# Kernel tuning notes

Hardware: AMD Instinct MI355X
Metric: run time of the kernel (lower is better)

## Reference

```python
import jax, jax.numpy as jnp
import numpy as np

RADIUS = 0.4
K = 32
EPS = 1e-5


def ball_query(xyz, new_xyz, radius, k):
    """xyz: (B,N,3), new_xyz: (B,M,3) -> idx (B,M,k) int32.
    Replicates CUDA ball_query: first k points within radius (in index order),
    padded with the first found index."""
    N = xyz.shape[1]
    # squared distances (B,M,N)
    d2 = jnp.sum((new_xyz[:, :, None, :] - xyz[:, None, :, :]) ** 2, axis=-1)
    within = d2 < radius * radius
    order = jnp.arange(N, dtype=jnp.int32)
    key = jnp.where(within, order[None, None, :], N)
    idx_sorted = jnp.argsort(key, axis=-1)[..., :k].astype(jnp.int32)  # (B,M,k)
    cnt = within.sum(axis=-1)  # (B,M)
    first = idx_sorted[..., :1]
    slot = jnp.arange(k)[None, None, :]
    return jnp.where(slot < cnt[..., None], idx_sorted, first)


def gather_bmk(x_bnc, idx):
    """x_bnc: (B,N,C), idx: (B,M,K) -> (B,M,K,C)"""
    return jnp.take_along_axis(x_bnc[:, None, :, :], idx[..., None], axis=2)


def conv_bn_relu(x, w, b, gamma, beta):
    """x: (B,Cin,M,K); w: (Cout,Cin). 1x1 Conv2d + BatchNorm2d (train stats) + ReLU."""
    x = jnp.einsum('bcmk,oc->bomk', x, w) + b[None, :, None, None]
    mu = x.mean(axis=(0, 2, 3), keepdims=True)
    var = x.var(axis=(0, 2, 3), keepdims=True)
    x = gamma[None, :, None, None] * (x - mu) * jax.lax.rsqrt(var + EPS) + beta[None, :, None, None]
    return jax.nn.relu(x)


def setup_inputs() -> dict:
    key = jax.random.key(0)
    ks = jax.random.split(key, 16)
    B, N, C, M = 4, 16384, 128, 1024
    mlp = [131, 128, 128, 256]
    inp = {
        'points_xyz': jax.random.normal(ks[0], (B, N, 3), dtype=jnp.float32),
        'features': jax.random.normal(ks[1], (B, C, N), dtype=jnp.float32),
        'indices': jax.random.randint(ks[2], (B, M), 0, N, dtype=jnp.int32),
    }
    for i in range(3):
        cin, cout = mlp[i], mlp[i + 1]
        inp[f'w{i+1}'] = jax.random.normal(ks[3 + 4 * i], (cout, cin), dtype=jnp.float32) / np.sqrt(cin)
        inp[f'b{i+1}'] = jnp.zeros((cout,), dtype=jnp.float32)
        inp[f'g{i+1}'] = jnp.ones((cout,), dtype=jnp.float32)
        inp[f'beta{i+1}'] = jnp.zeros((cout,), dtype=jnp.float32)
    return inp


def reference(points_xyz, features, indices,
              w1, b1, g1, beta1, w2, b2, g2, beta2, w3, b3, g3, beta3):
    # sample centers: new_xyz (B,M,3)
    new_xyz = jnp.take_along_axis(points_xyz, indices[..., None], axis=1)
    # ball query + group
    idx = ball_query(points_xyz, new_xyz, RADIUS, K)            # (B,M,K)
    grouped_xyz = gather_bmk(points_xyz, idx) - new_xyz[:, :, None, :]  # (B,M,K,3)
    grouped_feat = gather_bmk(features.transpose(0, 2, 1), idx)         # (B,M,K,C)
    x = jnp.concatenate([grouped_xyz, grouped_feat], axis=-1)           # (B,M,K,3+C)
    x = x.transpose(0, 3, 1, 2)                                         # (B,3+C,M,K)
    # shared MLP (1x1 Conv2d + BN + ReLU)
    x = conv_bn_relu(x, w1, b1, g1, beta1)
    x = conv_bn_relu(x, w2, b2, g2, beta2)
    x = conv_bn_relu(x, w3, b3, g3, beta3)
    # max pool over K -> (B, Cout, M)
    new_features = x.max(axis=-1)
    return new_xyz, new_features
```

## Files before the change

### kernel.cpp

```cpp
#include <hip/hip_runtime.h>

#define B_ 4
#define N_ 16384
#define C_ 128
#define M_ 1024
#define K_ 32
#define NTOT (B_*M_*K_)
#define RAD2 0.16f
#define EPS_ 1e-5f

typedef unsigned short ushort_t;
typedef __bf16 bf16x8 __attribute__((ext_vector_type(8)));
typedef float f32x4 __attribute__((ext_vector_type(4)));

__device__ __forceinline__ float b2f(ushort_t u){
  unsigned int x = ((unsigned int)u) << 16;
  return __builtin_bit_cast(float, x);
}
__device__ __forceinline__ ushort_t f2b(float f){
  return __builtin_bit_cast(ushort_t, (__bf16)f);
}

__global__ __launch_bounds__(256) void prep_all_k(
    const float* __restrict__ feat, ushort_t* __restrict__ ftr_t,
    const float* __restrict__ xyz, const int* __restrict__ indices,
    float* __restrict__ new_xyz, int* __restrict__ idx,
    const float* __restrict__ w1, const float* __restrict__ w2, const float* __restrict__ w3,
    ushort_t* __restrict__ W1b, ushort_t* __restrict__ W2b, ushort_t* __restrict__ W3b,
    float* __restrict__ stats)
{
  __shared__ float T[32][133];
  int bid = blockIdx.x;
  int t = threadIdx.x;

  if (bid < 1024){
    int wv = t >> 6, lane = t & 63;
    int g = bid*4 + wv;
    int b = g >> 10;
    const float* pb = xyz + (size_t)b*N_*3;
    const float4* pb4 = (const float4*)pb;
    int qi = indices[g];
    float qx = pb[qi*3+0], qy = pb[qi*3+1], qz = pb[qi*3+2];
    if (lane < 3) new_xyz[g*3 + lane] = pb[qi*3 + lane];

    int cnt = 0, firstIdx = 0;
    int* op = idx + g*K_;

    float4 buf0[6], buf1[6];
    #pragma unroll
    for (int i = 0; i < 6; i++) buf0[i] = pb4[lane*6 + i];

    unsigned long long below = (lane == 0) ? 0ull : ((~0ull) >> (64 - lane));

    auto process = [&](const float4* buf, int chunk){
      const float* f = (const float*)buf;
      unsigned int local_mask = 0;
      #pragma unroll
      for (int j = 0; j < 8; j++){
        float dx = f[j*3+0]-qx, dy = f[j*3+1]-qy, dz = f[j*3+2]-qz;
        if (dx*dx + dy*dy + dz*dz < RAD2) local_mask |= (1u << j);
      }
      unsigned long long many = __ballot(local_mask != 0);
      if (many == 0ull) return;
      int base = chunk*512;
      unsigned long long mj[8];
      #pragma unroll
      for (int j = 0; j < 8; j++) mj[j] = __ballot((local_mask >> j) & 1u);
      int excl = 0, total = 0;
      #pragma unroll
      for (int j = 0; j < 8; j++){
        excl  += __popcll(mj[j] & below);
        total += __popcll(mj[j]);
      }
      if (cnt == 0){
        int l0 = __builtin_ctzll(many);
        int j0 = 0;
        #pragma unroll
        for (int j = 7; j >= 0; j--) if ((mj[j] >> l0) & 1ull) j0 = j;
        firstIdx = base + l0*8 + j0;
      }
      int sl = cnt + excl;
      unsigned int m = local_mask;
      while (m && sl < K_){
        int j = __builtin_ctz(m); m &= m - 1u;
        op[sl++] = base + lane*8 + j;
      }
      cnt += total;
    };

    for (int chunk = 0; chunk < 32; chunk += 2){
      if (chunk + 1 < 32){
        #pragma unroll
        for (int i = 0; i < 6; i++) buf1[i] = pb4[(chunk+1)*384 + lane*6 + i];
      }
      process(buf0, chunk);
      if (cnt >= K_) break;
      if (chunk + 2 < 32){
        #pragma unroll
        for (int i = 0; i < 6; i++) buf0[i] = pb4[(chunk+2)*384 + lane*6 + i];
      }
      process(buf1, chunk + 1);
      if (cnt >= K_) break;
    }
    if (cnt < K_){
      for (int s = cnt + lane; s < K_; s += 64) op[s] = firstIdx;
    }
  } else if (bid < 3072){
    int bb = bid - 1024;
    int b = bb >> 9, ntile = bb & 511;
    int n0 = ntile * 32;
    int nl = t & 31;
    #pragma unroll
    for (int ci = 0; ci < 16; ci++){
      int c = ci*8 + (t >> 5);
      T[nl][c] = feat[((size_t)b*C_ + c)*N_ + n0 + nl];
    }
    __syncthreads();
    #pragma unroll
    for (int ii = 0; ii < 2; ii++){
      int v = ii*256 + t;
      int n2 = v >> 4, seg = v & 15;
      union { ushort_t u[8]; uint4 q; } pk;
      #pragma unroll
      for (int j = 0; j < 8; j++) pk.u[j] = f2b(T[n2][seg*8 + j]);
      *(uint4*)(ftr_t + ((size_t)b*N_ + n0 + n2)*C_ + seg*8) = pk.q;
    }
  } else {
    const int T1 = 128*160, T2 = 128*128;
    int e = (bid - 3072)*256 + t;
    if (e < T1){
      int o = e / 160, c = e % 160;
      float v = 0.f;
      if (c < 128) v = w1[o*131 + 3 + c];
      else if (c < 131) v = w1[o*131 + (c - 128)];
      W1b[e] = f2b(v);
    } else if (e < T1+T2){
      int e2 = e - T1;
      W2b[e2] = f2b(w2[e2]);
    } else {
      int e3 = e - T1 - T2;
      W3b[e3] = f2b(w3[e3]);
    }
    if (bid == 3072){
      #pragma unroll
      for (int j = 0; j < 6; j++) stats[j*256 + t] = 0.f;
    }
  }
}

__global__ __launch_bounds__(256, 4) void conv1_k(
    const float* __restrict__ xyz, const ushort_t* __restrict__ ftr_t,
    const int* __restrict__ idx, const float* __restrict__ new_xyz,
    const ushort_t* __restrict__ W1b, const float* __restrict__ b1,
    ushort_t* __restrict__ Y1, float* __restrict__ sumO, float* __restrict__ sqO)
{
  __shared__ alignas(16) ushort_t Xs[2][32*168];
  __shared__ alignas(16) float Ys[2][32*68];
  int t = threadIdx.x;
  int wv = t >> 6, lane = t & 63, quad = lane >> 4, l15 = lane & 15;
  int row = t >> 3, chunk = t & 7;
  int col0 = (blockIdx.x & 1) * 64;
  int blk = blockIdx.x >> 1;

  if (t < 128){
    int rr = t >> 2, cc = t & 3;
    *(uint4*)(Xs[0] + rr*168 + 128 + cc*8) = make_uint4(0,0,0,0);
    *(uint4*)(Xs[1] + rr*168 + 128 + cc*8) = make_uint4(0,0,0,0);
  }
  bf16x8 wf[5];
  #pragma unroll
  for (int kt = 0; kt < 5; kt++)
    wf[kt] = *(const bf16x8*)(W1b + (col0 + wv*16 + l15)*160 + kt*32 + quad*8);
  float bs_r = b1[col0 + wv*16 + l15];
  float s = 0.f, s2 = 0.f;

  const int GPB = 8;
  int g0 = blk * GPB;
  int b = g0 >> 10;
  int ia[GPB], ibv[GPB];
  #pragma unroll
  for (int i = 0; i < GPB; i++){
    ia[i]  = idx[(g0+i)*K_ + row];
    ibv[i] = idx[(g0+i)*K_ + (t & 31)];
  }
  uint4 r0, r1;
  float p3x, p3y, p3z, q3x, q3y, q3z;
  {
    const ushort_t* src = ftr_t + ((size_t)b*N_ + ia[0])*C_ + chunk*16;
    r0 = *(const uint4*)src; r1 = *(const uint4*)(src + 8);
    if (t < 32){
      const float* pp = xyz + ((size_t)b*N_ + ibv[0])*3;
      const float* qq = new_xyz + (size_t)g0*3;
      p3x = pp[0]; p3y = pp[1]; p3z = pp[2];
      q3x = qq[0]; q3y = qq[1]; q3z = qq[2];
    }
  }
  for (int i = 0; i < GPB; i++){
    int p = i & 1;
    ushort_t* X = Xs[p];
    *(uint4*)(X + row*168 + chunk*16) = r0;
    *(uint4*)(X + row*168 + chunk*16 + 8) = r1;
    if (t < 32){
      unsigned int u0 = (unsigned int)f2b(p3x-q3x) | ((unsigned int)f2b(p3y-q3y) << 16);
      unsigned int u1 = (unsigned int)f2b(p3z-q3z);
      *(uint2*)(X + t*168 + 128) = make_uint2(u0, u1);
    }
    if (i + 1 < GPB){
      const ushort_t* src = ftr_t + ((size_t)b*N_ + ia[i+1])*C_ + chunk*16;
      r0 = *(const uint4*)src; r1 = *(const uint4*)(src + 8);
      if (t < 32){
        const float* pp = xyz + ((size_t)b*N_ + ibv[i+1])*3;
        const float* qq = new_xyz + (size_t)(g0+i+1)*3;
        p3x = pp[0]; p3y = pp[1]; p3z = pp[2];
        q3x = qq[0]; q3y = qq[1]; q3z = qq[2];
      }
    }
    __syncthreads();
    bf16x8 af[2][5];
    #pragma unroll
    for (int mt = 0; mt < 2; mt++)
      #pragma unroll
      for (int kt = 0; kt < 5; kt++)
        af[mt][kt] = *(const bf16x8*)(X + (mt*16 + l15)*168 + kt*32 + quad*8);
    f32x4 acc[2] = {(f32x4){0,0,0,0}, (f32x4){0,0,0,0}};
    #pragma unroll
    for (int kt = 0; kt < 5; kt++){
      acc[0] = __builtin_amdgcn_mfma_f32_16x16x32_bf16(af[0][kt], wf[kt], acc[0], 0,0,0);
      acc[1] = __builtin_amdgcn_mfma_f32_16x16x32_bf16(af[1][kt], wf[kt], acc[1], 0,0,0);
    }
    {
      int o = wv*16 + l15;
      float* Yw = Ys[p];
      #pragma unroll
      for (int mt = 0; mt < 2; mt++)
        #pragma unroll
        for (int r = 0; r < 4; r++){
          float v = acc[mt][r] + bs_r;
          s += v; s2 += v*v;
          Yw[(mt*16 + quad*4 + r)*68 + o] = v;
        }
    }
    if (i > 0){
      const float* yp = &Ys[p^1][row*68 + chunk*8];
      f32x4 y0 = *(const f32x4*)(yp);
      f32x4 y1 = *(const f32x4*)(yp + 4);
      union { ushort_t u[8]; uint4 q; } p0;
      #pragma unroll
      for (int j = 0; j < 4; j++){
        p0.u[j] = f2b(y0[j]); p0.u[4+j] = f2b(y1[j]);
      }
      *(uint4*)(Y1 + ((size_t)(g0+i-1)*K_ + row)*128 + col0 + chunk*8) = p0.q;
    }
  }
  __syncthreads();
  {
    const float* yp = &Ys[(GPB-1)&1][row*68 + chunk*8];
    f32x4 y0 = *(const f32x4*)(yp);
    f32x4 y1 = *(const f32x4*)(yp + 4);
    union { ushort_t u[8]; uint4 q; } p0;
    #pragma unroll
    for (int j = 0; j < 4; j++){
      p0.u[j] = f2b(y0[j]); p0.u[4+j] = f2b(y1[j]);
    }
    *(uint4*)(Y1 + ((size_t)(g0+GPB-1)*K_ + row)*128 + col0 + chunk*8) = p0.q;
  }
  s  += __shfl_xor(s, 16);  s  += __shfl_xor(s, 32);
  s2 += __shfl_xor(s2, 16); s2 += __shfl_xor(s2, 32);
  if (quad == 0){
    int o = col0 + wv*16 + l15;
    atomicAdd(&sumO[o], s);
    atomicAdd(&sqO[o], s2);
  }
}

template<int COUT, bool MAXMIN, int MINB>
__global__ __launch_bounds__(256, MINB) void convB_k(
    const ushort_t* __restrict__ Yin, const ushort_t* __restrict__ Wb,
    const float* __restrict__ bias, const float* __restrict__ g_bn,
    const float* __restrict__ beta_bn, const float* __restrict__ sumI,
    const float* __restrict__ sqI, ushort_t* __restrict__ Yout,
    unsigned int* __restrict__ Ymm, float* __restrict__ sumO, float* __restrict__ sqO)
{
  constexpr int HALF = COUT/2;
  constexpr int NT = HALF/64;
  __shared__ alignas(16) ushort_t Xs[2][32*136];
  __shared__ alignas(16) float Ys[MAXMIN ? 1 : 2][MAXMIN ? 4 : 32*68];
  int t = threadIdx.x;
  int wv = t >> 6, lane = t & 63, quad = lane >> 4, l15 = lane & 15;
  int row = t >> 3, chunk = t & 7;
  int col0 = (blockIdx.x & 1) * HALF;
  int blk = blockIdx.x >> 1;

  float a_r[16], d_r[16];
  #pragma unroll
  for (int j = 0; j < 16; j++){
    int c = chunk*16 + j;
    float mu  = sumI[c] * (1.f/NTOT);
    float var = sqI[c]  * (1.f/NTOT) - mu*mu;
    float a = g_bn[c] * rsqrtf(var + EPS_);
    a_r[j] = a; d_r[j] = beta_bn[c] - a*mu;
  }
  bf16x8 wf[NT][4];
  #pragma unroll
  for (int nt = 0; nt < NT; nt++)
    #pragma unroll
    for (int kt = 0; kt < 4; kt++)
      wf[nt][kt] = *(const bf16x8*)(Wb + (col0 + wv*(NT*16) + nt*16 + l15)*128 + kt*32 + quad*8);
  float bs_r[NT];
  #pragma unroll
  for (int nt = 0; nt < NT; nt++) bs_r[nt] = bias[col0 + wv*(NT*16) + nt*16 + l15];
  float s[NT], s2[NT];
  #pragma unroll
  for (int nt = 0; nt < NT; nt++){ s[nt] = 0.f; s2[nt] = 0.f; }

  const int GPB = 8;
  int g0 = blk * GPB;
  uint4 r0, r1;
  {
    const ushort_t* src = Yin + ((size_t)g0*K_ + row)*128 + chunk*16;
    r0 = *(const uint4*)src; r1 = *(const uint4*)(src + 8);
  }
  for (int i = 0; i < GPB; i++){
    int p = i & 1;
    int g = g0 + i;
    ushort_t* X = Xs[p];
    union { ushort_t u[8]; uint4 q; } i0, i1, o0, o1;
    i0.q = r0; i1.q = r1;
    #pragma unroll
    for (int j = 0; j < 8; j++){
      o0.u[j] = f2b(fmaxf(a_r[j]  *b2f(i0.u[j]) + d_r[j],   0.f));
      o1.u[j] = f2b(fmaxf(a_r[8+j]*b2f(i1.u[j]) + d_r[8+j], 0.f));
    }
    *(uint4*)(X + row*136 + chunk*16) = o0.q;
    *(uint4*)(X + row*136 + chunk*16 + 8) = o1.q;
    if (i + 1 < GPB){
      const ushort_t* src = Yin + ((size_t)(g+1)*K_ + row)*128 + chunk*16;
      r0 = *(const uint4*)src; r1 = *(const uint4*)(src + 8);
    }
    __syncthreads();
    bf16x8 af[2][4];
    #pragma unroll
    for (int mt = 0; mt < 2; mt++)
      #pragma unroll
      for (int kt = 0; kt < 4; kt++)
        af[mt][kt] = *(const bf16x8*)(X + (mt*16 + l15)*136 + kt*32 + quad*8);
    f32x4 acc[NT][2];
    #pragma unroll
    for (int nt = 0; nt < NT; nt++){ acc[nt][0] = (f32x4){0,0,0,0}; acc[nt][1] = (f32x4){0,0,0,0}; }
    #pragma unroll
    for (int nt = 0; nt < NT; nt++)
      #pragma unroll
      for (int kt = 0; kt < 4; kt++){
        acc[nt][0] = __builtin_amdgcn_mfma_f32_16x16x32_bf16(af[0][kt], wf[nt][kt], acc[nt][0], 0,0,0);
        acc[nt][1] = __builtin_amdgcn_mfma_f32_16x16x32_bf16(af[1][kt], wf[nt][kt], acc[nt][1], 0,0,0);
      }
    if constexpr (!MAXMIN){
      {
        int o = wv*16 + l15;
        float* Yw = Ys[p];
        #pragma unroll
        for (int mt = 0; mt < 2; mt++)
          #pragma unroll
          for (int r = 0; r < 4; r++){
            float v = acc[0][mt][r] + bs_r[0];
            s[0] += v; s2[0] += v*v;
            Yw[(mt*16 + quad*4 + r)*68 + o] = v;
          }
      }
      if (i > 0){
        const float* yp = &Ys[p^1][row*68 + chunk*8];
        f32x4 y0 = *(const f32x4*)(yp);
        f32x4 y1 = *(const f32x4*)(yp + 4);
        union { ushort_t u[8]; uint4 q; } p0;
        #pragma unroll
        for (int j = 0; j < 4; j++){
          p0.u[j] = f2b(y0[j]); p0.u[4+j] = f2b(y1[j]);
        }
        *(uint4*)(Yout + ((size_t)(g-1)*K_ + row)*128 + col0 + chunk*8) = p0.q;
      }
    } else {
      #pragma unroll
      for (int nt = 0; nt < NT; nt++){
        float v0 = acc[nt][0][0] + bs_r[nt];
        float mx = v0, mn = v0;
        s[nt] += v0; s2[nt] += v0*v0;
        #pragma unroll
        for (int mt = 0; mt < 2; mt++)
          #pragma unroll
          for (int r = 0; r < 4; r++){
            if (mt == 0 && r == 0) continue;
            float v = acc[nt][mt][r] + bs_r[nt];
            s[nt] += v; s2[nt] += v*v;
            mx = fmaxf(mx, v); mn = fminf(mn, v);
          }
        mx = fmaxf(mx, __shfl_xor(mx, 16)); mx = fmaxf(mx, __shfl_xor(mx, 32));
        mn = fminf(mn, __shfl_xor(mn, 16)); mn = fminf(mn, __shfl_xor(mn, 32));
        if (quad == 0){
          int o = col0 + wv*(NT*16) + nt*16 + l15;
          Ymm[(size_t)g*256 + o] = (unsigned int)f2b(mx) | ((unsigned int)f2b(mn) << 16);
        }
      }
    }
  }
  if constexpr (!MAXMIN){
    __syncthreads();
    const float* yp = &Ys[(GPB-1)&1][row*68 + chunk*8];
    f32x4 y0 = *(const f32x4*)(yp);
    f32x4 y1 = *(const f32x4*)(yp + 4);
    union { ushort_t u[8]; uint4 q; } p0;
    #pragma unroll
    for (int j = 0; j < 4; j++){
      p0.u[j] = f2b(y0[j]); p0.u[4+j] = f2b(y1[j]);
    }
    *(uint4*)(Yout + ((size_t)(g0+GPB-1)*K_ + row)*128 + col0 + chunk*8) = p0.q;
  }
  #pragma unroll
  for (int nt = 0; nt < NT; nt++){
    s[nt]  += __shfl_xor(s[nt], 16);  s[nt]  += __shfl_xor(s[nt], 32);
    s2[nt] += __shfl_xor(s2[nt], 16); s2[nt] += __shfl_xor(s2[nt], 32);
    if (quad == 0){
      int o = col0 + wv*(NT*16) + nt*16 + l15;
      atomicAdd(&sumO[o], s[nt]);
      atomicAdd(&sqO[o], s2[nt]);
    }
  }
}

__global__ __launch_bounds__(256) void finalize_k(
    const unsigned int* __restrict__ Ymm, const float* __restrict__ g3,
    const float* __restrict__ beta3, const float* __restrict__ sum3,
    const float* __restrict__ sq3, float* __restrict__ out)
{
  __shared__ float T[16][264];
  __shared__ float abn[256], dbn[256];
  int t = threadIdx.x;
  int b = blockIdx.x >> 6;
  int m0 = (blockIdx.x & 63) * 16;
  {
    float mu  = sum3[t] * (1.f/NTOT);
    float var = sq3[t]  * (1.f/NTOT) - mu*mu;
    float a = g3[t] * rsqrtf(var + EPS_);
    abn[t] = a; dbn[t] = beta3[t] - a*mu;
  }
  __syncthreads();
  #pragma unroll
  for (int i = 0; i < 4; i++){
    int v4 = i*256 + t;
    int m = v4 >> 6, oq = (v4 & 63) * 4;
    uint4 w = *(const uint4*)(Ymm + ((size_t)(b*M_ + m0 + m))*256 + oq);
    unsigned int wsv[4] = {w.x, w.y, w.z, w.w};
    float r[4];
    #pragma unroll
    for (int j = 0; j < 4; j++){
      int o = oq + j;
      float mx = b2f((ushort_t)(wsv[j] & 0xffffu));
      float mn = b2f((ushort_t)(wsv[j] >> 16));
      float a = abn[o];
      float val = (a >= 0.f) ? (a*mx + dbn[o]) : (a*mn + dbn[o]);
      r[j] = fmaxf(val, 0.f);
    }
    *(f32x4*)(&T[m][oq]) = *(f32x4*)r;
  }
  __syncthreads();
  #pragma unroll
  for (int p = 0; p < 4; p++){
    int o = p*64 + (t >> 2), c = t & 3;
    float4 v = make_float4(T[c*4+0][o], T[c*4+1][o], T[c*4+2][o], T[c*4+3][o]);
    *(float4*)(out + ((size_t)(b*256 + o))*M_ + m0 + c*4) = v;
  }
}

extern "C" void kernel_launch(void* const* d_in, const int* in_sizes, int n_in,
                              void* d_out, int out_size, void* d_ws, size_t ws_size,
                              hipStream_t stream)
{
  (void)in_sizes; (void)n_in; (void)out_size; (void)ws_size;
  const float* xyz  = (const float*)d_in[0];
  const float* feat = (const float*)d_in[1];
  const int*   inds = (const int*)d_in[2];
  const float* w1 = (const float*)d_in[3];
  const float* b1 = (const float*)d_in[4];
  const float* g1 = (const float*)d_in[5];
  const float* be1= (const float*)d_in[6];
  const float* w2 = (const float*)d_in[7];
  const float* b2 = (const float*)d_in[8];
  const float* g2 = (const float*)d_in[9];
  const float* be2= (const float*)d_in[10];
  const float* w3 = (const float*)d_in[11];
  const float* b3 = (const float*)d_in[12];
  const float* g3 = (const float*)d_in[13];
  const float* be3= (const float*)d_in[14];

  char* ws = (char*)d_ws;
  float* stats = (float*)ws;
  float* s1sum = stats + 0*256;  float* s1sq = stats + 1*256;
  float* s2sum = stats + 2*256;  float* s2sq = stats + 3*256;
  float* s3sum = stats + 4*256;  float* s3sq = stats + 5*256;
  size_t off = 6*256*sizeof(float);
  int* idx = (int*)(ws + off);                off += (size_t)B_*M_*K_*4;
  ushort_t* ftr_t = (ushort_t*)(ws + off);    off += (size_t)B_*N_*C_*2;
  ushort_t* W1b = (ushort_t*)(ws + off);      off += 128*160*2;
  ushort_t* W2b = (ushort_t*)(ws + off);      off += 128*128*2;
  ushort_t* W3b = (ushort_t*)(ws + off);      off += 256*128*2;
  ushort_t* Y1 = (ushort_t*)(ws + off);       off += (size_t)NTOT*128*2;
  ushort_t* Y2 = (ushort_t*)(ws + off);       off += (size_t)NTOT*128*2;
  unsigned int* Ymm = (unsigned int*)(ws + off); off += (size_t)B_*M_*256*4;

  float* new_xyz  = (float*)d_out;
  float* out_feat = (float*)d_out + (size_t)B_*M_*3;

  prep_all_k<<<3344, 256, 0, stream>>>(feat, ftr_t, xyz, inds, new_xyz, idx,
                                       w1, w2, w3, W1b, W2b, W3b, stats);
  conv1_k<<<1024, 256, 0, stream>>>(xyz, ftr_t, idx, new_xyz, W1b, b1, Y1, s1sum, s1sq);
  convB_k<128,false,4><<<1024, 256, 0, stream>>>(Y1, W2b, b2, g1, be1, s1sum, s1sq, Y2, nullptr, s2sum, s2sq);
  convB_k<256,true ,3><<<1024, 256, 0, stream>>>(Y2, W3b, b3, g2, be2, s2sum, s2sq, nullptr, Ymm, s3sum, s3sq);
  finalize_k<<<256, 256, 0, stream>>>(Ymm, g3, be3, s3sum, s3sq, out_feat);
}
```

Measured before the change: 211.6 us.

## Store conv2 output in MFMA fragment layout and split conv2/conv3 kernels

Conv2 now computes all 128 output channels per block over 4 groups and writes its results straight from MFMA accumulators in a fragment-native layout. This drops the LDS staging buffer and the transpose pass that came before the global write. Conv3 reads that layout and rebuilds the row-major LDS tile with per-channel-pair BN+ReLU, then keeps the max/min epilogue. The aim is to cut LDS traffic and syncs in conv2, at the cost of narrower scattered 8-byte stores and more scattered LDS writes in conv3.

```diff
diff --git a/kernel.cpp b/kernel.cpp
--- a/kernel.cpp
+++ b/kernel.cpp
@@ -273,23 +273,18 @@
   }
 }
 
-template<int COUT, bool MAXMIN, int MINB>
-__global__ __launch_bounds__(256, MINB) void convB_k(
+__global__ __launch_bounds__(256, 4) void conv2_k(
     const ushort_t* __restrict__ Yin, const ushort_t* __restrict__ Wb,
     const float* __restrict__ bias, const float* __restrict__ g_bn,
     const float* __restrict__ beta_bn, const float* __restrict__ sumI,
-    const float* __restrict__ sqI, ushort_t* __restrict__ Yout,
-    unsigned int* __restrict__ Ymm, float* __restrict__ sumO, float* __restrict__ sqO)
+    const float* __restrict__ sqI, ushort_t* __restrict__ Yf,
+    float* __restrict__ sumO, float* __restrict__ sqO)
 {
-  constexpr int HALF = COUT/2;
-  constexpr int NT = HALF/64;
   __shared__ alignas(16) ushort_t Xs[2][32*136];
-  __shared__ alignas(16) float Ys[MAXMIN ? 1 : 2][MAXMIN ? 4 : 32*68];
   int t = threadIdx.x;
   int wv = t >> 6, lane = t & 63, quad = lane >> 4, l15 = lane & 15;
   int row = t >> 3, chunk = t & 7;
-  int col0 = (blockIdx.x & 1) * HALF;
-  int blk = blockIdx.x >> 1;
+  int blk = blockIdx.x;
 
   float a_r[16], d_r[16];
   #pragma unroll
@@ -300,20 +295,18 @@
     float a = g_bn[c] * rsqrtf(var + EPS_);
     a_r[j] = a; d_r[j] = beta_bn[c] - a*mu;
   }
-  bf16x8 wf[NT][4];
-  #pragma unroll
-  for (int nt = 0; nt < NT; nt++)
+  bf16x8 wf[2][4];
+  #pragma unroll
+  for (int nt = 0; nt < 2; nt++)
     #pragma unroll
     for (int kt = 0; kt < 4; kt++)
-      wf[nt][kt] = *(const bf16x8*)(Wb + (col0 + wv*(NT*16) + nt*16 + l15)*128 + kt*32 + quad*8);
-  float bs_r[NT];
-  #pragma unroll
-  for (int nt = 0; nt < NT; nt++) bs_r[nt] = bias[col0 + wv*(NT*16) + nt*16 + l15];
-  float s[NT], s2[NT];
-  #pragma unroll
-  for (int nt = 0; nt < NT; nt++){ s[nt] = 0.f; s2[nt] = 0.f; }
-
-  const int GPB = 8;
+      wf[nt][kt] = *(const bf16x8*)(Wb + (wv*32 + nt*16 + l15)*128 + kt*32 + quad*8);
+  float bs_r[2];
+  #pragma unroll
+  for (int nt = 0; nt < 2; nt++) bs_r[nt] = bias[wv*32 + nt*16 + l15];
+  float s[2] = {0.f, 0.f}, s2[2] = {0.f, 0.f};
+
+  const int GPB = 4;
   int g0 = blk * GPB;
   uint4 r0, r1;
   {
@@ -338,88 +331,152 @@
       r0 = *(const uint4*)src; r1 = *(const uint4*)(src + 8);
     }
     __syncthreads();
-    bf16x8 af[2][4];
-    #pragma unroll
-    for (int mt = 0; mt < 2; mt++)
-      #pragma unroll
-      for (int kt = 0; kt < 4; kt++)
-        af[mt][kt] = *(const bf16x8*)(X + (mt*16 + l15)*136 + kt*32 + quad*8);
-    f32x4 acc[NT][2];
-    #pragma unroll
-    for (int nt = 0; nt < NT; nt++){ acc[nt][0] = (f32x4){0,0,0,0}; acc[nt][1] = (f32x4){0,0,0,0}; }
-    #pragma unroll
-    for (int nt = 0; nt < NT; nt++)
-      #pragma unroll
-      for (int kt = 0; kt < 4; kt++){
-        acc[nt][0] = __builtin_amdgcn_mfma_f32_16x16x32_bf16(af[0][kt], wf[nt][kt], acc[nt][0], 0,0,0);
-        acc[nt][1] = __builtin_amdgcn_mfma_f32_16x16x32_bf16(af[1][kt], wf[nt][kt], acc[nt][1], 0,0,0);
-      }
-    if constexpr (!MAXMIN){
-      {
-        int o = wv*16 + l15;
-        float* Yw = Ys[p];
-        #pragma unroll
-        for (int mt = 0; mt < 2; mt++)
-          #pragma unroll
-          for (int r = 0; r < 4; r++){
-            float v = acc[0][mt][r] + bs_r[0];
-            s[0] += v; s2[0] += v*v;
-            Yw[(mt*16 + quad*4 + r)*68 + o] = v;
-          }
-      }
-      if (i > 0){
-        const float* yp = &Ys[p^1][row*68 + chunk*8];
-        f32x4 y0 = *(const f32x4*)(yp);
-        f32x4 y1 = *(const f32x4*)(yp + 4);
-        union { ushort_t u[8]; uint4 q; } p0;
-        #pragma unroll
-        for (int j = 0; j < 4; j++){
-          p0.u[j] = f2b(y0[j]); p0.u[4+j] = f2b(y1[j]);
-        }
-        *(uint4*)(Yout + ((size_t)(g-1)*K_ + row)*128 + col0 + chunk*8) = p0.q;
-      }
-    } else {
-      #pragma unroll
-      for (int nt = 0; nt < NT; nt++){
-        float v0 = acc[nt][0][0] + bs_r[nt];
-        float mx = v0, mn = v0;
-        s[nt] += v0; s2[nt] += v0*v0;
-        #pragma unroll
-        for (int mt = 0; mt < 2; mt++)
-          #pragma unroll
-          for (int r = 0; r < 4; r++){
-            if (mt == 0 && r == 0) continue;
-            float v = acc[nt][mt][r] + bs_r[nt];
-            s[nt] += v; s2[nt] += v*v;
-            mx = fmaxf(mx, v); mn = fminf(mn, v);
-          }
-        mx = fmaxf(mx, __shfl_xor(mx, 16)); mx = fmaxf(mx, __shfl_xor(mx, 32));
-        mn = fminf(mn, __shfl_xor(mn, 16)); mn = fminf(mn, __shfl_xor(mn, 32));
-        if (quad == 0){
-          int o = col0 + wv*(NT*16) + nt*16 + l15;
-          Ymm[(size_t)g*256 + o] = (unsigned int)f2b(mx) | ((unsigned int)f2b(mn) << 16);
-        }
-      }
-    }
-  }
-  if constexpr (!MAXMIN){
-    __syncthreads();
-    const float* yp = &Ys[(GPB-1)&1][row*68 + chunk*8];
-    f32x4 y0 = *(const f32x4*)(yp);
-    f32x4 y1 = *(const f32x4*)(yp + 4);
-    union { ushort_t u[8]; uint4 q; } p0;
-    #pragma unroll
-    for (int j = 0; j < 4; j++){
-      p0.u[j] = f2b(y0[j]); p0.u[4+j] = f2b(y1[j]);
-    }
-    *(uint4*)(Yout + ((size_t)(g0+GPB-1)*K_ + row)*128 + col0 + chunk*8) = p0.q;
-  }
-  #pragma unroll
-  for (int nt = 0; nt < NT; nt++){
+    f32x4 acc[2][2];
+    acc[0][0] = (f32x4){0,0,0,0}; acc[0][1] = (f32x4){0,0,0,0};
+    acc[1][0] = (f32x4){0,0,0,0}; acc[1][1] = (f32x4){0,0,0,0};
+    #pragma unroll
+    for (int kt = 0; kt < 4; kt++){
+      bf16x8 A0 = *(const bf16x8*)(X + (l15)*136      + kt*32 + quad*8);
+      bf16x8 A1 = *(const bf16x8*)(X + (16 + l15)*136 + kt*32 + quad*8);
+      acc[0][0] = __builtin_amdgcn_mfma_f32_16x16x32_bf16(A0, wf[0][kt], acc[0][0], 0,0,0);
+      acc[0][1] = __builtin_amdgcn_mfma_f32_16x16x32_bf16(A1, wf[0][kt], acc[0][1], 0,0,0);
+      acc[1][0] = __builtin_amdgcn_mfma_f32_16x16x32_bf16(A0, wf[1][kt], acc[1][0], 0,0,0);
+      acc[1][1] = __builtin_amdgcn_mfma_f32_16x16x32_bf16(A1, wf[1][kt], acc[1][1], 0,0,0);
+    }
+    #pragma unroll
+    for (int nt = 0; nt < 2; nt++){
+      #pragma unroll
+      for (int mt = 0; mt < 2; mt++){
+        float v0 = acc[nt][mt][0] + bs_r[nt];
+        float v1 = acc[nt][mt][1] + bs_r[nt];
+        float v2 = acc[nt][mt][2] + bs_r[nt];
+        float v3 = acc[nt][mt][3] + bs_r[nt];
+        s[nt]  += v0 + v1 + v2 + v3;
+        s2[nt] += v0*v0 + v1*v1 + v2*v2 + v3*v3;
+        uint2 w;
+        w.x = (unsigned int)f2b(v0) | ((unsigned int)f2b(v1) << 16);
+        w.y = (unsigned int)f2b(v2) | ((unsigned int)f2b(v3) << 16);
+        size_t seg = ((size_t)g*2 + mt)*8 + (wv*2 + nt);
+        *(uint2*)(Yf + seg*256 + (quad*16 + l15)*4) = w;
+      }
+    }
+  }
+  #pragma unroll
+  for (int nt = 0; nt < 2; nt++){
     s[nt]  += __shfl_xor(s[nt], 16);  s[nt]  += __shfl_xor(s[nt], 32);
     s2[nt] += __shfl_xor(s2[nt], 16); s2[nt] += __shfl_xor(s2[nt], 32);
     if (quad == 0){
-      int o = col0 + wv*(NT*16) + nt*16 + l15;
+      int o = wv*32 + nt*16 + l15;
+      atomicAdd(&sumO[o], s[nt]);
+      atomicAdd(&sqO[o], s2[nt]);
+    }
+  }
+}
+
+__global__ __launch_bounds__(256, 4) void conv3_k(
+    const ushort_t* __restrict__ Yf, const ushort_t* __restrict__ Wb,
+    const float* __restrict__ bias, const float* __restrict__ g_bn,
+    const float* __restrict__ beta_bn, const float* __restrict__ sumI,
+    const float* __restrict__ sqI,
+    unsigned int* __restrict__ Ymm, float* __restrict__ sumO, float* __restrict__ sqO)
+{
+  __shared__ alignas(16) ushort_t Xs[2][32*136];
+  int t = threadIdx.x;
+  int wv = t >> 6, lane = t & 63, quad = lane >> 4, l15 = lane & 15;
+  int col0 = (blockIdx.x & 1) * 128;
+  int blk = blockIdx.x >> 1;
+
+  int rest = t & 255;
+  int sseg = rest >> 5, q = (rest >> 3) & 3, pr = rest & 7;
+  int c0 = sseg*16 + pr*2;
+  float A0c, D0c, A1c, D1c;
+  {
+    float mu0  = sumI[c0] * (1.f/NTOT);
+    float var0 = sqI[c0]  * (1.f/NTOT) - mu0*mu0;
+    A0c = g_bn[c0] * rsqrtf(var0 + EPS_);
+    D0c = beta_bn[c0] - A0c*mu0;
+    float mu1  = sumI[c0+1] * (1.f/NTOT);
+    float var1 = sqI[c0+1]  * (1.f/NTOT) - mu1*mu1;
+    A1c = g_bn[c0+1] * rsqrtf(var1 + EPS_);
+    D1c = beta_bn[c0+1] - A1c*mu1;
+  }
+  bf16x8 wf[2][4];
+  #pragma unroll
+  for (int nt = 0; nt < 2; nt++)
+    #pragma unroll
+    for (int kt = 0; kt < 4; kt++)
+      wf[nt][kt] = *(const bf16x8*)(Wb + (col0 + wv*32 + nt*16 + l15)*128 + kt*32 + quad*8);
+  float bs_r[2];
+  #pragma unroll
+  for (int nt = 0; nt < 2; nt++) bs_r[nt] = bias[col0 + wv*32 + nt*16 + l15];
+  float s[2] = {0.f, 0.f}, s2[2] = {0.f, 0.f};
+
+  const int GPB = 8;
+  int g0 = blk * GPB;
+  int finner = sseg*256 + q*64 + pr*8;
+  uint4 r0, r1;
+  r0 = *(const uint4*)(Yf + ((size_t)g0*2 + 0)*2048 + finner);
+  r1 = *(const uint4*)(Yf + ((size_t)g0*2 + 1)*2048 + finner);
+  for (int i = 0; i < GPB; i++){
+    int p = i & 1;
+    int g = g0 + i;
+    ushort_t* X = Xs[p];
+    union { ushort_t u[8]; uint4 q4; } i0, i1;
+    i0.q4 = r0; i1.q4 = r1;
+    #pragma unroll
+    for (int r = 0; r < 4; r++){
+      unsigned int w0 = (unsigned int)f2b(fmaxf(A0c*b2f(i0.u[r])   + D0c, 0.f))
+                      | ((unsigned int)f2b(fmaxf(A1c*b2f(i0.u[4+r]) + D1c, 0.f)) << 16);
+      unsigned int w1 = (unsigned int)f2b(fmaxf(A0c*b2f(i1.u[r])   + D0c, 0.f))
+                      | ((unsigned int)f2b(fmaxf(A1c*b2f(i1.u[4+r]) + D1c, 0.f)) << 16);
+      *(unsigned int*)(X + (q*4 + r)*136 + c0)      = w0;
+      *(unsigned int*)(X + (16 + q*4 + r)*136 + c0) = w1;
+    }
+    if (i + 1 < GPB){
+      r0 = *(const uint4*)(Yf + ((size_t)(g+1)*2 + 0)*2048 + finner);
+      r1 = *(const uint4*)(Yf + ((size_t)(g+1)*2 + 1)*2048 + finner);
+    }
+    __syncthreads();
+    f32x4 acc[2][2];
+    acc[0][0] = (f32x4){0,0,0,0}; acc[0][1] = (f32x4){0,0,0,0};
+    acc[1][0] = (f32x4){0,0,0,0}; acc[1][1] = (f32x4){0,0,0,0};
+    #pragma unroll
+    for (int kt = 0; kt < 4; kt++){
+      bf16x8 A0 = *(const bf16x8*)(X + (l15)*136      + kt*32 + quad*8);
+      bf16x8 A1 = *(const bf16x8*)(X + (16 + l15)*136 + kt*32 + quad*8);
+      acc[0][0] = __builtin_amdgcn_mfma_f32_16x16x32_bf16(A0, wf[0][kt], acc[0][0], 0,0,0);
+      acc[0][1] = __builtin_amdgcn_mfma_f32_16x16x32_bf16(A1, wf[0][kt], acc[0][1], 0,0,0);
+      acc[1][0] = __builtin_amdgcn_mfma_f32_16x16x32_bf16(A0, wf[1][kt], acc[1][0], 0,0,0);
+      acc[1][1] = __builtin_amdgcn_mfma_f32_16x16x32_bf16(A1, wf[1][kt], acc[1][1], 0,0,0);
+    }
+    #pragma unroll
+    for (int nt = 0; nt < 2; nt++){
+      float v0 = acc[nt][0][0] + bs_r[nt];
+      float mx = v0, mn = v0;
+      s[nt] += v0; s2[nt] += v0*v0;
+      #pragma unroll
+      for (int mt = 0; mt < 2; mt++)
+        #pragma unroll
+        for (int r = 0; r < 4; r++){
+          if (mt == 0 && r == 0) continue;
+          float v = acc[nt][mt][r] + bs_r[nt];
+          s[nt] += v; s2[nt] += v*v;
+          mx = fmaxf(mx, v); mn = fminf(mn, v);
+        }
+      mx = fmaxf(mx, __shfl_xor(mx, 16)); mx = fmaxf(mx, __shfl_xor(mx, 32));
+      mn = fminf(mn, __shfl_xor(mn, 16)); mn = fminf(mn, __shfl_xor(mn, 32));
+      if (quad == 0){
+        int o = col0 + wv*32 + nt*16 + l15;
+        Ymm[(size_t)g*256 + o] = (unsigned int)f2b(mx) | ((unsigned int)f2b(mn) << 16);
+      }
+    }
+  }
+  #pragma unroll
+  for (int nt = 0; nt < 2; nt++){
+    s[nt]  += __shfl_xor(s[nt], 16);  s[nt]  += __shfl_xor(s[nt], 32);
+    s2[nt] += __shfl_xor(s2[nt], 16); s2[nt] += __shfl_xor(s2[nt], 32);
+    if (quad == 0){
+      int o = col0 + wv*32 + nt*16 + l15;
       atomicAdd(&sumO[o], s[nt]);
       atomicAdd(&sqO[o], s2[nt]);
     }
@@ -512,7 +569,7 @@
   prep_all_k<<<3344, 256, 0, stream>>>(feat, ftr_t, xyz, inds, new_xyz, idx,
                                        w1, w2, w3, W1b, W2b, W3b, stats);
   conv1_k<<<1024, 256, 0, stream>>>(xyz, ftr_t, idx, new_xyz, W1b, b1, Y1, s1sum, s1sq);
-  convB_k<128,false,4><<<1024, 256, 0, stream>>>(Y1, W2b, b2, g1, be1, s1sum, s1sq, Y2, nullptr, s2sum, s2sq);
-  convB_k<256,true ,3><<<1024, 256, 0, stream>>>(Y2, W3b, b3, g2, be2, s2sum, s2sq, nullptr, Ymm, s3sum, s3sq);
+  conv2_k<<<1024, 256, 0, stream>>>(Y1, W2b, b2, g1, be1, s1sum, s1sq, Y2, s2sum, s2sq);
+  conv3_k<<<1024, 256, 0, stream>>>(Y2, W3b, b3, g2, be2, s2sum, s2sq, Ymm, s3sum, s3sq);
   finalize_k<<<256, 256, 0, stream>>>(Ymm, g3, be3, s3sum, s3sq, out_feat);
 }
```

Result: slower. 220.2 us (+4.1%).

## Stage ball-query points through shared memory in SoA layout shared by block

Applied to the files above, without the earlier changes.

The ball-query block now loads each 512-point chunk once cooperatively into a double-buffered SoA shared-memory arena, instead of each wave loading its own float4 slices from global memory. The four waves in a block share the xyz chunks and synchronize each step, leaving the loop together once all waves have found K neighbors. Point assignment now interleaves lanes (point j*64+lane), and the per-lane output loop is replaced by a per-bit prefix scheme. This cuts redundant global loads across waves, but adds block-wide barriers that make early-finishing waves wait for the slowest one.

```diff
diff --git a/kernel.cpp b/kernel.cpp
--- a/kernel.cpp
+++ b/kernel.cpp
@@ -38,69 +38,82 @@
     int g = bid*4 + wv;
     int b = g >> 10;
     const float* pb = xyz + (size_t)b*N_*3;
-    const float4* pb4 = (const float4*)pb;
     int qi = indices[g];
     float qx = pb[qi*3+0], qy = pb[qi*3+1], qz = pb[qi*3+2];
     if (lane < 3) new_xyz[g*3 + lane] = pb[qi*3 + lane];
 
     int cnt = 0, firstIdx = 0;
     int* op = idx + g*K_;
-
-    float4 buf0[6], buf1[6];
-    #pragma unroll
-    for (int i = 0; i < 6; i++) buf0[i] = pb4[lane*6 + i];
-
     unsigned long long below = (lane == 0) ? 0ull : ((~0ull) >> (64 - lane));
 
-    auto process = [&](const float4* buf, int chunk){
-      const float* f = (const float*)buf;
+    float* arena = &T[0][0];
+    int sp[6], sc[6];
+    #pragma unroll
+    for (int k = 0; k < 6; k++){
+      int f = t + k*256;
+      sp[k] = f / 3; sc[k] = f - sp[k]*3;
+    }
+
+    float ld[6];
+    auto stageLoad = [&](int c){
+      const float* src = pb + c*1536;
+      #pragma unroll
+      for (int k = 0; k < 6; k++) ld[k] = src[t + k*256];
+    };
+    auto stageWrite = [&](int buf){
+      float* A = arena + buf*1536;
+      #pragma unroll
+      for (int k = 0; k < 6; k++) A[sc[k]*512 + sp[k]] = ld[k];
+    };
+
+    auto process = [&](int buf, int c){
+      const float* AX = arena + buf*1536;
+      const float* AY = AX + 512;
+      const float* AZ = AY + 512;
       unsigned int local_mask = 0;
       #pragma unroll
       for (int j = 0; j < 8; j++){
-        float dx = f[j*3+0]-qx, dy = f[j*3+1]-qy, dz = f[j*3+2]-qz;
+        int p = j*64 + lane;
+        float dx = AX[p]-qx, dy = AY[p]-qy, dz = AZ[p]-qz;
         if (dx*dx + dy*dy + dz*dz < RAD2) local_mask |= (1u << j);
       }
       unsigned long long many = __ballot(local_mask != 0);
       if (many == 0ull) return;
-      int base = chunk*512;
+      int base = c*512;
       unsigned long long mj[8];
       #pragma unroll
       for (int j = 0; j < 8; j++) mj[j] = __ballot((local_mask >> j) & 1u);
-      int excl = 0, total = 0;
+      if (cnt == 0){
+        int j0 = 7;
+        #pragma unroll
+        for (int j = 7; j >= 0; j--) if (mj[j] != 0ull) j0 = j;
+        firstIdx = base + j0*64 + __builtin_ctzll(mj[j0]);
+      }
+      int pref = 0;
       #pragma unroll
       for (int j = 0; j < 8; j++){
-        excl  += __popcll(mj[j] & below);
-        total += __popcll(mj[j]);
-      }
-      if (cnt == 0){
-        int l0 = __builtin_ctzll(many);
-        int j0 = 0;
-        #pragma unroll
-        for (int j = 7; j >= 0; j--) if ((mj[j] >> l0) & 1ull) j0 = j;
-        firstIdx = base + l0*8 + j0;
-      }
-      int sl = cnt + excl;
-      unsigned int m = local_mask;
-      while (m && sl < K_){
-        int j = __builtin_ctz(m); m &= m - 1u;
-        op[sl++] = base + lane*8 + j;
-      }
-      cnt += total;
+        if ((local_mask >> j) & 1u){
+          int sl = cnt + pref + __popcll(mj[j] & below);
+          if (sl < K_) op[sl] = base + j*64 + lane;
+        }
+        pref += __popcll(mj[j]);
+      }
+      cnt += pref;
     };
 
-    for (int chunk = 0; chunk < 32; chunk += 2){
-      if (chunk + 1 < 32){
-        #pragma unroll
-        for (int i = 0; i < 6; i++) buf1[i] = pb4[(chunk+1)*384 + lane*6 + i];
-      }
-      process(buf0, chunk);
-      if (cnt >= K_) break;
-      if (chunk + 2 < 32){
-        #pragma unroll
-        for (int i = 0; i < 6; i++) buf0[i] = pb4[(chunk+2)*384 + lane*6 + i];
-      }
-      process(buf1, chunk + 1);
-      if (cnt >= K_) break;
+    stageLoad(0);
+    stageWrite(0);
+    __syncthreads();
+    bool wdone = false;
+    for (int c = 0; c < 32; c++){
+      bool have_next = (c + 1 < 32);
+      if (have_next) stageLoad(c + 1);
+      if (!wdone){
+        process(c & 1, c);
+        if (cnt >= K_) wdone = true;
+      }
+      if (have_next) stageWrite((c + 1) & 1);
+      if (__syncthreads_and((int)wdone)) break;
     }
     if (cnt < K_){
       for (int s = cnt + lane; s < K_; s += 64) op[s] = firstIdx;
```

Result: slower. 219.3 us (+3.6%).

## Add dedicated conv2 kernel covering all 128 output channels per block

Applied to the files above, without the earlier changes.

Replaces the generic convB kernel for layer 2 with a specialised kernel where each block computes all 128 output channels for 4 groups. Each wave keeps a 32-channel weight slice in registers and loads, normalises and activates the input tile once, where the generic kernel appears to split output channels into halves. Group processing is double-buffered in shared memory, so the next group's input load and the previous group's bf16 output store overlap with the current MFMA work. The cost is more registers and shared memory per block, which may reduce occupancy.

```diff
diff --git a/kernel.cpp b/kernel.cpp
--- a/kernel.cpp
+++ b/kernel.cpp
@@ -270,6 +270,142 @@
     int o = col0 + wv*16 + l15;
     atomicAdd(&sumO[o], s);
     atomicAdd(&sqO[o], s2);
+  }
+}
+
+__global__ __launch_bounds__(256, 3) void conv2_k(
+    const ushort_t* __restrict__ Yin, const ushort_t* __restrict__ Wb,
+    const float* __restrict__ bias, const float* __restrict__ g_bn,
+    const float* __restrict__ beta_bn, const float* __restrict__ sumI,
+    const float* __restrict__ sqI, ushort_t* __restrict__ Yout,
+    float* __restrict__ sumO, float* __restrict__ sqO)
+{
+  __shared__ alignas(16) ushort_t Xs[2][32*136];
+  __shared__ alignas(16) float Ys[2][32*132];
+  int t = threadIdx.x;
+  int wv = t >> 6, lane = t & 63, quad = lane >> 4, l15 = lane & 15;
+  int row = t >> 3, chunk = t & 7;
+  int blk = blockIdx.x;
+
+  float a_r[16], d_r[16];
+  #pragma unroll
+  for (int j = 0; j < 16; j++){
+    int c = chunk*16 + j;
+    float mu  = sumI[c] * (1.f/NTOT);
+    float var = sqI[c]  * (1.f/NTOT) - mu*mu;
+    float a = g_bn[c] * rsqrtf(var + EPS_);
+    a_r[j] = a; d_r[j] = beta_bn[c] - a*mu;
+  }
+  bf16x8 wf[2][4];
+  #pragma unroll
+  for (int nt = 0; nt < 2; nt++)
+    #pragma unroll
+    for (int kt = 0; kt < 4; kt++)
+      wf[nt][kt] = *(const bf16x8*)(Wb + (wv*32 + nt*16 + l15)*128 + kt*32 + quad*8);
+  float bs_r[2];
+  #pragma unroll
+  for (int nt = 0; nt < 2; nt++) bs_r[nt] = bias[wv*32 + nt*16 + l15];
+  float s[2] = {0.f, 0.f}, s2[2] = {0.f, 0.f};
+
+  const int GPB = 4;
+  int g0 = blk * GPB;
+  uint4 r0, r1;
+  {
+    const ushort_t* src = Yin + ((size_t)g0*K_ + row)*128 + chunk*16;
+    r0 = *(const uint4*)src; r1 = *(const uint4*)(src + 8);
+  }
+  for (int i = 0; i < GPB; i++){
+    int p = i & 1;
+    int g = g0 + i;
+    ushort_t* X = Xs[p];
+    union { ushort_t u[8]; uint4 q; } i0, i1, o0, o1;
+    i0.q = r0; i1.q = r1;
+    #pragma unroll
+    for (int j = 0; j < 8; j++){
+      o0.u[j] = f2b(fmaxf(a_r[j]  *b2f(i0.u[j]) + d_r[j],   0.f));
+      o1.u[j] = f2b(fmaxf(a_r[8+j]*b2f(i1.u[j]) + d_r[8+j], 0.f));
+    }
+    *(uint4*)(X + row*136 + chunk*16) = o0.q;
+    *(uint4*)(X + row*136 + chunk*16 + 8) = o1.q;
+    if (i + 1 < GPB){
+      const ushort_t* src = Yin + ((size_t)(g+1)*K_ + row)*128 + chunk*16;
+      r0 = *(const uint4*)src; r1 = *(const uint4*)(src + 8);
+    }
+    __syncthreads();
+    bf16x8 af[2][4];
+    #pragma unroll
+    for (int mt = 0; mt < 2; mt++)
+      #pragma unroll
+      for (int kt = 0; kt < 4; kt++)
+        af[mt][kt] = *(const bf16x8*)(X + (mt*16 + l15)*136 + kt*32 + quad*8);
+    f32x4 acc[2][2];
+    acc[0][0] = (f32x4){0,0,0,0}; acc[0][1] = (f32x4){0,0,0,0};
+    acc[1][0] = (f32x4){0,0,0,0}; acc[1][1] = (f32x4){0,0,0,0};
+    #pragma unroll
+    for (int kt = 0; kt < 4; kt++){
+      acc[0][0] = __builtin_amdgcn_mfma_f32_16x16x32_bf16(af[0][kt], wf[0][kt], acc[0][0], 0,0,0);
+      acc[0][1] = __builtin_amdgcn_mfma_f32_16x16x32_bf16(af[1][kt], wf[0][kt], acc[0][1], 0,0,0);
+      acc[1][0] = __builtin_amdgcn_mfma_f32_16x16x32_bf16(af[0][kt], wf[1][kt], acc[1][0], 0,0,0);
+      acc[1][1] = __builtin_amdgcn_mfma_f32_16x16x32_bf16(af[1][kt], wf[1][kt], acc[1][1], 0,0,0);
+    }
+    {
+      float* Yw = Ys[p];
+      #pragma unroll
+      for (int nt = 0; nt < 2; nt++){
+        int o = wv*32 + nt*16 + l15;
+        #pragma unroll
+        for (int mt = 0; mt < 2; mt++)
+          #pragma unroll
+          for (int r = 0; r < 4; r++){
+            float v = acc[nt][mt][r] + bs_r[nt];
+            s[nt] += v; s2[nt] += v*v;
+            Yw[(mt*16 + quad*4 + r)*132 + o] = v;
+          }
+      }
+    }
+    if (i > 0){
+      const float* yp = &Ys[p^1][row*132 + chunk*16];
+      f32x4 y0 = *(const f32x4*)(yp);
+      f32x4 y1 = *(const f32x4*)(yp + 4);
+      f32x4 y2 = *(const f32x4*)(yp + 8);
+      f32x4 y3 = *(const f32x4*)(yp + 12);
+      union { ushort_t u[16]; uint4 q[2]; } p0;
+      #pragma unroll
+      for (int j = 0; j < 4; j++){
+        p0.u[j]    = f2b(y0[j]); p0.u[4+j]  = f2b(y1[j]);
+        p0.u[8+j]  = f2b(y2[j]); p0.u[12+j] = f2b(y3[j]);
+      }
+      ushort_t* dst = Yout + ((size_t)(g-1)*K_ + row)*128 + chunk*16;
+      *(uint4*)dst = p0.q[0];
+      *(uint4*)(dst + 8) = p0.q[1];
+    }
+  }
+  __syncthreads();
+  {
+    const float* yp = &Ys[(GPB-1)&1][row*132 + chunk*16];
+    f32x4 y0 = *(const f32x4*)(yp);
+    f32x4 y1 = *(const f32x4*)(yp + 4);
+    f32x4 y2 = *(const f32x4*)(yp + 8);
+    f32x4 y3 = *(const f32x4*)(yp + 12);
+    union { ushort_t u[16]; uint4 q[2]; } p0;
+    #pragma unroll
+    for (int j = 0; j < 4; j++){
+      p0.u[j]    = f2b(y0[j]); p0.u[4+j]  = f2b(y1[j]);
+      p0.u[8+j]  = f2b(y2[j]); p0.u[12+j] = f2b(y3[j]);
+    }
+    ushort_t* dst = Yout + ((size_t)(g0+GPB-1)*K_ + row)*128 + chunk*16;
+    *(uint4*)dst = p0.q[0];
+    *(uint4*)(dst + 8) = p0.q[1];
+  }
+  #pragma unroll
+  for (int nt = 0; nt < 2; nt++){
+    s[nt]  += __shfl_xor(s[nt], 16);  s[nt]  += __shfl_xor(s[nt], 32);
+    s2[nt] += __shfl_xor(s2[nt], 16); s2[nt] += __shfl_xor(s2[nt], 32);
+    if (quad == 0){
+      int o = wv*32 + nt*16 + l15;
+      atomicAdd(&sumO[o], s[nt]);
+      atomicAdd(&sqO[o], s2[nt]);
+    }
   }
 }
 
@@ -512,7 +648,7 @@
   prep_all_k<<<3344, 256, 0, stream>>>(feat, ftr_t, xyz, inds, new_xyz, idx,
                                        w1, w2, w3, W1b, W2b, W3b, stats);
   conv1_k<<<1024, 256, 0, stream>>>(xyz, ftr_t, idx, new_xyz, W1b, b1, Y1, s1sum, s1sq);
-  convB_k<128,false,4><<<1024, 256, 0, stream>>>(Y1, W2b, b2, g1, be1, s1sum, s1sq, Y2, nullptr, s2sum, s2sq);
+  conv2_k<<<1024, 256, 0, stream>>>(Y1, W2b, b2, g1, be1, s1sum, s1sq, Y2, s2sum, s2sq);
   convB_k<256,true ,3><<<1024, 256, 0, stream>>>(Y2, W3b, b3, g2, be2, s2sum, s2sq, nullptr, Ymm, s3sum, s3sq);
   finalize_k<<<256, 256, 0, stream>>>(Ymm, g3, be3, s3sum, s3sq, out_feat);
 }
```

Result: slower. 217.8 us (+2.9%).
